# Kernel tuning notes

Measured on AMD Instinct MI355X. Metric: run time of the kernel, lower is better.

## Reference

```python
import jax, jax.numpy as jnp
import numpy as np

B, N, NINP, NFEAT, H = 4096, 4096, 64, 32, 4


def setup_inputs() -> dict:
    key = jax.random.key(0)
    ks = jax.random.split(key, 8)
    s_in = 1.0 / np.sqrt(NINP)
    s_att = 1.0 / np.sqrt(2 * NFEAT)
    return {
        "X": jax.random.normal(ks[0], (B, NINP), jnp.float32),
        "G": jax.random.normal(ks[1], (N, NINP), jnp.float32),
        "A": jax.random.uniform(ks[2], (B, N), jnp.float32),  # additive mask
        "W": jax.random.uniform(ks[3], (H, NINP, NFEAT), jnp.float32, -s_in, s_in),
        "b": jax.random.uniform(ks[4], (H, NFEAT), jnp.float32, -s_in, s_in),
        "a_src": jax.random.uniform(ks[5], (H, NFEAT), jnp.float32, -s_att, s_att),
        "a_dst": jax.random.uniform(ks[6], (H, NFEAT), jnp.float32, -s_att, s_att),
        "att_b": jax.random.uniform(ks[7], (H,), jnp.float32, -s_att, s_att),
    }


def reference(X, G, A, W, b, a_src, a_dst, att_b):
    # Per-head linear transforms (all heads batched via einsum)
    WX = jnp.einsum("bi,hif->bhf", X, W) + b            # (B, H, F)
    WG = jnp.einsum("ni,hif->nhf", G, W) + b            # (N, H, F)
    # Decomposed concat-attention: a^T [WX_b ; WG_n] = a_src.WX_b + a_dst.WG_n
    s_src = jnp.einsum("bhf,hf->bh", WX, a_src)         # (B, H)
    s_dst = jnp.einsum("nhf,hf->nh", WG, a_dst)         # (N, H)
    e = s_src[:, :, None] + s_dst.T[None, :, :] + att_b[None, :, None]  # (B,H,N)
    att = jax.nn.softmax(e - A[:, None, :], axis=-1)    # adjacency-masked softmax
    # Dropout(0.5) is identity in eval mode (deterministic reference).
    out = jnp.einsum("bhn,nhf->bhf", att, WG)           # weighted aggregation
    out = jax.nn.relu(out)                              # activation before concat
    return out.reshape(out.shape[0], -1)                # (B, H*F) concat heads
```

## Files before the change

### kernel.cpp

```cpp
#include <hip/hip_runtime.h>
#include <stdint.h>

#define N_TOK 4096
#define D_IN  64
#define NF    32
#define NH    4
#define OUTW  (NH * NF)
#define NT    8
#define CHUNK 128
#define BT    32

typedef float        f32x4  __attribute__((ext_vector_type(4)));
typedef unsigned int uint4v __attribute__((ext_vector_type(4)));
typedef __bf16       bf16x8 __attribute__((ext_vector_type(8)));

union Frag { uint4v u; bf16x8 v; };

static __device__ __forceinline__ unsigned short f2bf_rne(float x) {
  unsigned u = __float_as_uint(x);
  u += 0x7fffu + ((u >> 16) & 1u);
  return (unsigned short)(u >> 16);
}

__global__ __launch_bounds__(128) void prep_kernel(
    const float* __restrict__ G, const float* __restrict__ W,
    const float* __restrict__ bias, const float* __restrict__ a_dst,
    unsigned short* __restrict__ PB) {
  __shared__ float gs[NT * D_IN];
  const int tid = threadIdx.x;
  const int n0  = blockIdx.x * NT;
  {
    const float4* src = (const float4*)(G + (size_t)n0 * D_IN);
    float4* dst = (float4*)gs;
    dst[tid] = src[tid];
  }
  __syncthreads();
  const int h = tid >> 5, f = tid & 31;
  float acc[NT];
  const float bb = bias[h * NF + f];
#pragma unroll
  for (int k = 0; k < NT; ++k) acc[k] = bb;
#pragma unroll
  for (int i = 0; i < D_IN; ++i) {
    const float wv = W[(h * D_IN + i) * NF + f];
#pragma unroll
    for (int k = 0; k < NT; ++k) acc[k] = fmaf(gs[k * D_IN + i], wv, acc[k]);
  }
  const float ad = a_dst[h * NF + f];
  float ev[NT];
#pragma unroll
  for (int k = 0; k < NT; ++k) {
    float s = acc[k] * ad;
    s += __shfl_xor(s, 1);  s += __shfl_xor(s, 2);  s += __shfl_xor(s, 4);
    s += __shfl_xor(s, 8);  s += __shfl_xor(s, 16);
    ev[k] = __expf(s);
  }
  const int t   = n0 >> 5;
  const int gq  = (n0 >> 3) & 3;
  const int set = (h << 1) | (f >> 4);
  const int col = f & 31 & 15;
  union { uint4 u4; unsigned short us[8]; } pk;
#pragma unroll
  for (int k = 0; k < NT; ++k) pk.us[k] = f2bf_rne(acc[k] * ev[k]);
  *(uint4*)(PB + (size_t)((((t * 9 + set) << 6) + (gq << 4) + col)) * 8) = pk.u4;
  if (f == 0) {
    union { uint4 u4; unsigned short us[8]; } pe;
#pragma unroll
    for (int k = 0; k < NT; ++k) pe.us[k] = f2bf_rne(ev[k]);
    *(uint4*)(PB + (size_t)((((t * 9 + 8) << 6) + (gq << 4) + h)) * 8) = pe.u4;
  }
  if (h == 0 && f >= 4 && f < 16) {
    uint4 z; z.x = 0u; z.y = 0u; z.z = 0u; z.w = 0u;
    *(uint4*)(PB + (size_t)((((t * 9 + 8) << 6) + (gq << 4) + f)) * 8) = z;
  }
}

template <int NS>
__global__ __launch_bounds__(512) void attn_kernel(
    const float* __restrict__ A, const unsigned short* __restrict__ PB,
    float* __restrict__ op, float* __restrict__ dp, float* __restrict__ out) {
  constexpr int NHALF  = N_TOK / NS;
  constexpr int NIT    = NHALF / CHUNK;
  constexpr int RINGSZ = BT * CHUNK * 2;
  __shared__ __align__(16) unsigned short ring[3 * BT * CHUNK];
  char* ringb = (char*)ring;

  const int tid  = threadIdx.x;
  const int lane = tid & 63;
  const int w    = tid >> 6;
  const int bid  = blockIdx.x;
  const int s    = bid & (NS - 1);
  const int b0   = (bid / NS) * BT;

  const int srow = tid >> 4, tp = tid & 15;
  const float* abase = A + (size_t)(b0 + srow) * N_TOK + s * NHALF + tp * 8;
  const int wb0 = srow * 256 + ((tp ^ (srow & 15)) << 4);

  const int rowm = lane & 15, g = lane >> 4;
  const char* pbb  = (const char*)PB + (size_t)s * (NHALF / 32) * 9216;
  const char* pown = pbb + (((w << 6) + lane) << 4);
  const char* pden = pbb + (((8 << 6) + lane) << 4);

  f32x4 acc0  = {0.f, 0.f, 0.f, 0.f}, acc1  = {0.f, 0.f, 0.f, 0.f};
  f32x4 accd0 = {0.f, 0.f, 0.f, 0.f}, accd1 = {0.f, 0.f, 0.f, 0.f};
  f32x4 aXa, aXb, aYa, aYb;
  Frag bo0, bo1, bo2, bo3, bd0, bd1, bd2, bd3;
  Frag co0, co1, co2, co3, cd0, cd1, cd2, cd3;
  int mR = 0, mW = 1;

#define LOADA2(d0, d1, cc) do {                                                \
    const float* ap_ = abase + (size_t)(cc) * CHUNK;                           \
    asm volatile("global_load_dwordx4 %0, %1, off"                            \
                 : "=v"(d0) : "v"(ap_) : "memory");                            \
    asm volatile("global_load_dwordx4 %0, %1, off"                            \
                 : "=v"(d1) : "v"(ap_ + 4) : "memory");                        \
  } while (0)
#define LOADBO(fr, cc, kk)                                                     \
  asm volatile("global_load_dwordx4 %0, %1, off"                              \
               : "=v"(fr.u)                                                    \
               : "v"(pown + (size_t)((cc) * 4 + (kk)) * 9216) : "memory")
#define LOADBD(fr, cc, kk)                                                     \
  asm volatile("global_load_dwordx4 %0, %1, off"                              \
               : "=v"(fr.u)                                                    \
               : "v"(pden + (size_t)((cc) * 4 + (kk)) * 9216) : "memory")

#define EXPP(AV0, AV1, mw) do {                                                \
    float x0 = __expf(-AV0[0]), x1 = __expf(-AV0[1]);                          \
    float x2 = __expf(-AV0[2]), x3 = __expf(-AV0[3]);                          \
    float x4 = __expf(-AV1[0]), x5 = __expf(-AV1[1]);                          \
    float x6 = __expf(-AV1[2]), x7 = __expf(-AV1[3]);                          \
    uint4v t_;                                                                 \
    t_[0] = __builtin_amdgcn_perm(__float_as_uint(x1), __float_as_uint(x0), 0x07060302u); \
    t_[1] = __builtin_amdgcn_perm(__float_as_uint(x3), __float_as_uint(x2), 0x07060302u); \
    t_[2] = __builtin_amdgcn_perm(__float_as_uint(x5), __float_as_uint(x4), 0x07060302u); \
    t_[3] = __builtin_amdgcn_perm(__float_as_uint(x7), __float_as_uint(x6), 0x07060302u); \
    *(uint4v*)(ringb + (mw) * RINGSZ + wb0) = t_;                              \
  } while (0)

#define MSTEP(rg, kk, FB, FD) do {                                             \
    Frag af_;                                                                  \
    af_.v = *(const bf16x8*)(ringb + mR * RINGSZ + ((rg) * 16 + rowm) * 256 +  \
                             ((((kk) * 4 + g) ^ rowm) << 4));                  \
    if ((rg) == 0) {                                                           \
      acc0  = __builtin_amdgcn_mfma_f32_16x16x32_bf16(af_.v, FB.v, acc0,  0, 0, 0); \
      accd0 = __builtin_amdgcn_mfma_f32_16x16x32_bf16(af_.v, FD.v, accd0, 0, 0, 0); \
    } else {                                                                   \
      acc1  = __builtin_amdgcn_mfma_f32_16x16x32_bf16(af_.v, FB.v, acc1,  0, 0, 0); \
      accd1 = __builtin_amdgcn_mfma_f32_16x16x32_bf16(af_.v, FD.v, accd1, 0, 0, 0); \
    }                                                                          \
  } while (0)

#define ITER(cc, AC0, AC1, AN0, AN1, CO0, CO1, CO2, CO3, CD0, CD1, CD2, CD3,   \
             NO0, NO1, NO2, NO3, ND0, ND1, ND2, ND3) do {                      \
    { const int cb_ = ((cc) + 1 < NIT) ? (cc) + 1 : NIT - 1;                   \
      LOADBO(NO0, cb_, 0); LOADBO(NO1, cb_, 1);                                \
      LOADBO(NO2, cb_, 2); LOADBO(NO3, cb_, 3);                                \
      LOADBD(ND0, cb_, 0); LOADBD(ND1, cb_, 1);                                \
      LOADBD(ND2, cb_, 2); LOADBD(ND3, cb_, 3); }                              \
    { const int ca_ = ((cc) + 2 < NIT) ? (cc) + 2 : NIT - 1;                   \
      LOADA2(AN0, AN1, ca_); }                                                 \
    asm volatile("s_waitcnt vmcnt(10)" ::: "memory");                          \
    __builtin_amdgcn_sched_barrier(0);                                         \
    EXPP(AC0, AC1, mW);                                                        \
    asm volatile("s_waitcnt lgkmcnt(0)" ::: "memory");                         \
    __builtin_amdgcn_sched_barrier(0);                                         \
    __builtin_amdgcn_s_barrier();                                              \
    MSTEP(0, 0, CO0, CD0); MSTEP(1, 0, CO0, CD0);                              \
    MSTEP(0, 1, CO1, CD1); MSTEP(1, 1, CO1, CD1);                              \
    MSTEP(0, 2, CO2, CD2); MSTEP(1, 2, CO2, CD2);                              \
    MSTEP(0, 3, CO3, CD3); MSTEP(1, 3, CO3, CD3);                              \
    mR = mW; mW = (mW + 1 == 3) ? 0 : mW + 1;                                  \
  } while (0)

  LOADA2(aXa, aXb, 0);
  LOADBO(bo0, 0, 0); LOADBO(bo1, 0, 1); LOADBO(bo2, 0, 2); LOADBO(bo3, 0, 3);
  LOADBD(bd0, 0, 0); LOADBD(bd1, 0, 1); LOADBD(bd2, 0, 2); LOADBD(bd3, 0, 3);
  LOADA2(aYa, aYb, 1);
  asm volatile("s_waitcnt vmcnt(10)" ::: "memory");
  __builtin_amdgcn_sched_barrier(0);
  EXPP(aXa, aXb, 0);

#pragma unroll 1
  for (int i = 0; i < NIT; i += 2) {
    ITER(i,     aYa, aYb, aXa, aXb, bo0, bo1, bo2, bo3, bd0, bd1, bd2, bd3,
                                    co0, co1, co2, co3, cd0, cd1, cd2, cd3);
    ITER(i + 1, aXa, aXb, aYa, aYb, co0, co1, co2, co3, cd0, cd1, cd2, cd3,
                                    bo0, bo1, bo2, bo3, bd0, bd1, bd2, bd3);
  }

  asm volatile("s_waitcnt vmcnt(0)" ::: "memory");
  __builtin_amdgcn_sched_barrier(0);

  if (NS == 1) {
    const int hh = w >> 1;
#pragma unroll
    for (int r = 0; r < 4; ++r) {
      const float dn0 = __shfl(accd0[r], g * 16 + hh);
      const float o0 = acc0[r] / dn0;
      out[(size_t)(b0 + g * 4 + r) * OUTW + w * 16 + rowm] = o0 > 0.f ? o0 : 0.f;
      const float dn1 = __shfl(accd1[r], g * 16 + hh);
      const float o1 = acc1[r] / dn1;
      out[(size_t)(b0 + 16 + g * 4 + r) * OUTW + w * 16 + rowm] = o1 > 0.f ? o1 : 0.f;
    }
  } else {
    float* ob = op + (size_t)s * (N_TOK * OUTW) + (size_t)b0 * OUTW + w * 16 + rowm;
#pragma unroll
    for (int r = 0; r < 4; ++r) {
      ob[(size_t)(g * 4 + r) * OUTW]      = acc0[r];
      ob[(size_t)(16 + g * 4 + r) * OUTW] = acc1[r];
    }
    if (w == 0 && rowm < NH) {
#pragma unroll
      for (int r = 0; r < 4; ++r) {
        dp[((size_t)s * N_TOK + b0 + g * 4 + r) * NH + rowm]      = accd0[r];
        dp[((size_t)s * N_TOK + b0 + 16 + g * 4 + r) * NH + rowm] = accd1[r];
      }
    }
  }
#undef LOADA2
#undef LOADBO
#undef LOADBD
#undef EXPP
#undef MSTEP
#undef ITER
}

__global__ __launch_bounds__(256) void comb_kernel(
    const float* __restrict__ op, const float* __restrict__ dp,
    float* __restrict__ out, int NS) {
  const int idx4 = blockIdx.x * 256 + threadIdx.x;
  const int eb = idx4 >> 5;
  const int h  = ((idx4 << 2) & 127) >> 5;
  float4 o; o.x = 0.f; o.y = 0.f; o.z = 0.f; o.w = 0.f;
  float d = 0.f;
  for (int s2 = 0; s2 < NS; ++s2) {
    float4 vv = *(const float4*)(op + (size_t)s2 * (N_TOK * OUTW) + (size_t)idx4 * 4);
    o.x += vv.x; o.y += vv.y; o.z += vv.z; o.w += vv.w;
    d += dp[((size_t)s2 * N_TOK + eb) * NH + h];
  }
  const float r = 1.f / d;
  float4 res;
  res.x = fmaxf(o.x * r, 0.f);
  res.y = fmaxf(o.y * r, 0.f);
  res.z = fmaxf(o.z * r, 0.f);
  res.w = fmaxf(o.w * r, 0.f);
  *(float4*)(out + (size_t)idx4 * 4) = res;
}

extern "C" void kernel_launch(void* const* d_in, const int* in_sizes, int n_in,
                              void* d_out, int out_size, void* d_ws, size_t ws_size,
                              hipStream_t stream) {
  const float* G     = (const float*)d_in[1];
  const float* A     = (const float*)d_in[2];
  const float* W     = (const float*)d_in[3];
  const float* bias  = (const float*)d_in[4];
  const float* a_dst = (const float*)d_in[6];

  char* ws = (char*)d_ws;
  const size_t PBsz = (size_t)128 * 9 * 1024;
  const size_t per_split = (size_t)N_TOK * OUTW * 4 + (size_t)N_TOK * NH * 4;

  unsigned short* PB = (unsigned short*)ws;
  float* op = (float*)(ws + PBsz);
  float* outp = (float*)d_out;

  prep_kernel<<<N_TOK / NT, 128, 0, stream>>>(G, W, bias, a_dst, PB);
  if (ws_size >= PBsz + 4 * per_split) {
    float* dp = (float*)(ws + PBsz + 4 * (size_t)N_TOK * OUTW * 4);
    attn_kernel<4><<<(N_TOK / BT) * 4, 512, 0, stream>>>(A, PB, op, dp, nullptr);
    comb_kernel<<<(N_TOK * OUTW / 4) / 256, 256, 0, stream>>>(op, dp, outp, 4);
  } else if (ws_size >= PBsz + 2 * per_split) {
    float* dp = (float*)(ws + PBsz + 2 * (size_t)N_TOK * OUTW * 4);
    attn_kernel<2><<<(N_TOK / BT) * 2, 512, 0, stream>>>(A, PB, op, dp, nullptr);
    comb_kernel<<<(N_TOK * OUTW / 4) / 256, 256, 0, stream>>>(op, dp, outp, 2);
  } else {
    attn_kernel<1><<<N_TOK / BT, 512, 0, stream>>>(A, PB, nullptr, nullptr, outp);
  }
}
```

Baseline: 34.04 us.

## Compute softmax denominators with VALU FMAs instead of extra MFMAs

Removes the denominator MFMA path (4 extra global fragment loads and 8 extra MFMAs per chunk per wave). The per-head exp(s_dst) values are instead staged in LDS once per block, and each thread accumulates the denominator with scalar FMAs during the exp stage. The accumulation is then reduced via shuffles. This shrinks PB traffic and MFMA work, but adds 32 FMAs per thread per chunk, an LDS prologue copy, and extra LDS usage that could affect occupancy.

```diff
diff --git a/kernel.cpp b/kernel.cpp
--- a/kernel.cpp
+++ b/kernel.cpp
@@ -21,11 +21,17 @@
   u += 0x7fffu + ((u >> 16) & 1u);
   return (unsigned short)(u >> 16);
 }
+static __device__ __forceinline__ float bflo(unsigned x) {
+  return __uint_as_float(x << 16);
+}
+static __device__ __forceinline__ float bfhi(unsigned x) {
+  return __uint_as_float(x & 0xffff0000u);
+}
 
 __global__ __launch_bounds__(128) void prep_kernel(
     const float* __restrict__ G, const float* __restrict__ W,
     const float* __restrict__ bias, const float* __restrict__ a_dst,
-    unsigned short* __restrict__ PB) {
+    unsigned short* __restrict__ EDH, unsigned short* __restrict__ PB) {
   __shared__ float gs[NT * D_IN];
   const int tid = threadIdx.x;
   const int n0  = blockIdx.x * NT;
@@ -58,31 +64,30 @@
   const int t   = n0 >> 5;
   const int gq  = (n0 >> 3) & 3;
   const int set = (h << 1) | (f >> 4);
-  const int col = f & 31 & 15;
+  const int col = f & 15;
   union { uint4 u4; unsigned short us[8]; } pk;
 #pragma unroll
   for (int k = 0; k < NT; ++k) pk.us[k] = f2bf_rne(acc[k] * ev[k]);
-  *(uint4*)(PB + (size_t)((((t * 9 + set) << 6) + (gq << 4) + col)) * 8) = pk.u4;
+  *(uint4*)(PB + (size_t)((((t * 8 + set) << 6) + (gq << 4) + col)) * 8) = pk.u4;
   if (f == 0) {
     union { uint4 u4; unsigned short us[8]; } pe;
 #pragma unroll
     for (int k = 0; k < NT; ++k) pe.us[k] = f2bf_rne(ev[k]);
-    *(uint4*)(PB + (size_t)((((t * 9 + 8) << 6) + (gq << 4) + h)) * 8) = pe.u4;
-  }
-  if (h == 0 && f >= 4 && f < 16) {
-    uint4 z; z.x = 0u; z.y = 0u; z.z = 0u; z.w = 0u;
-    *(uint4*)(PB + (size_t)((((t * 9 + 8) << 6) + (gq << 4) + f)) * 8) = z;
+    *(uint4*)&EDH[(size_t)h * N_TOK + n0] = pe.u4;
   }
 }
 
 template <int NS>
 __global__ __launch_bounds__(512) void attn_kernel(
-    const float* __restrict__ A, const unsigned short* __restrict__ PB,
-    float* __restrict__ op, float* __restrict__ dp, float* __restrict__ out) {
+    const float* __restrict__ A, const unsigned short* __restrict__ EDH,
+    const unsigned short* __restrict__ PB, float* __restrict__ op,
+    float* __restrict__ dp, float* __restrict__ out) {
   constexpr int NHALF  = N_TOK / NS;
   constexpr int NIT    = NHALF / CHUNK;
   constexpr int RINGSZ = BT * CHUNK * 2;
   __shared__ __align__(16) unsigned short ring[3 * BT * CHUNK];
+  __shared__ __align__(16) unsigned short EDt[NH * NHALF];
+  __shared__ float denLds[BT * NH];
   char* ringb = (char*)ring;
 
   const int tid  = threadIdx.x;
@@ -97,15 +102,25 @@
   const int wb0 = srow * 256 + ((tp ^ (srow & 15)) << 4);
 
   const int rowm = lane & 15, g = lane >> 4;
-  const char* pbb  = (const char*)PB + (size_t)s * (NHALF / 32) * 9216;
+  const char* pbb  = (const char*)PB + (size_t)s * (NHALF / 32) * 8192;
   const char* pown = pbb + (((w << 6) + lane) << 4);
-  const char* pden = pbb + (((8 << 6) + lane) << 4);
-
-  f32x4 acc0  = {0.f, 0.f, 0.f, 0.f}, acc1  = {0.f, 0.f, 0.f, 0.f};
-  f32x4 accd0 = {0.f, 0.f, 0.f, 0.f}, accd1 = {0.f, 0.f, 0.f, 0.f};
+
+  {
+    const uint4* src = (const uint4*)EDH;
+    uint4* dst = (uint4*)EDt;
+    constexpr int tot = NH * NHALF / 8;
+#pragma unroll 1
+    for (int i = tid; i < tot; i += 512) {
+      const int hh = i / (NHALF / 8), k = i % (NHALF / 8);
+      dst[i] = src[hh * (N_TOK / 8) + s * (NHALF / 8) + k];
+    }
+  }
+  __syncthreads();
+
+  f32x4 acc0 = {0.f, 0.f, 0.f, 0.f}, acc1 = {0.f, 0.f, 0.f, 0.f};
+  f32x4 dsum = {0.f, 0.f, 0.f, 0.f};
   f32x4 aXa, aXb, aYa, aYb;
-  Frag bo0, bo1, bo2, bo3, bd0, bd1, bd2, bd3;
-  Frag co0, co1, co2, co3, cd0, cd1, cd2, cd3;
+  Frag bo0, bo1, bo2, bo3, co0, co1, co2, co3;
   int mR = 0, mW = 1;
 
 #define LOADA2(d0, d1, cc) do {                                                \
@@ -115,20 +130,55 @@
     asm volatile("global_load_dwordx4 %0, %1, off"                            \
                  : "=v"(d1) : "v"(ap_ + 4) : "memory");                        \
   } while (0)
-#define LOADBO(fr, cc, kk)                                                     \
+#define LOADB(fr, cc, kk)                                                      \
   asm volatile("global_load_dwordx4 %0, %1, off"                              \
                : "=v"(fr.u)                                                    \
-               : "v"(pown + (size_t)((cc) * 4 + (kk)) * 9216) : "memory")
-#define LOADBD(fr, cc, kk)                                                     \
-  asm volatile("global_load_dwordx4 %0, %1, off"                              \
-               : "=v"(fr.u)                                                    \
-               : "v"(pden + (size_t)((cc) * 4 + (kk)) * 9216) : "memory")
-
-#define EXPP(AV0, AV1, mw) do {                                                \
+               : "v"(pown + (size_t)((cc) * 4 + (kk)) * 8192) : "memory")
+
+#define EXPP(AV0, AV1, cchunk, mw) do {                                        \
     float x0 = __expf(-AV0[0]), x1 = __expf(-AV0[1]);                          \
     float x2 = __expf(-AV0[2]), x3 = __expf(-AV0[3]);                          \
     float x4 = __expf(-AV1[0]), x5 = __expf(-AV1[1]);                          \
     float x6 = __expf(-AV1[2]), x7 = __expf(-AV1[3]);                          \
+    if ((cchunk) < NIT) {                                                      \
+      const int eo_ = (cchunk) * CHUNK + tp * 8;                               \
+      uint4v e0_ = *(const uint4v*)&EDt[0 * NHALF + eo_];                      \
+      uint4v e1_ = *(const uint4v*)&EDt[1 * NHALF + eo_];                      \
+      uint4v e2_ = *(const uint4v*)&EDt[2 * NHALF + eo_];                      \
+      uint4v e3_ = *(const uint4v*)&EDt[3 * NHALF + eo_];                      \
+      dsum[0] = fmaf(x0, bflo(e0_[0]), dsum[0]);                               \
+      dsum[0] = fmaf(x1, bfhi(e0_[0]), dsum[0]);                               \
+      dsum[0] = fmaf(x2, bflo(e0_[1]), dsum[0]);                               \
+      dsum[0] = fmaf(x3, bfhi(e0_[1]), dsum[0]);                               \
+      dsum[0] = fmaf(x4, bflo(e0_[2]), dsum[0]);                               \
+      dsum[0] = fmaf(x5, bfhi(e0_[2]), dsum[0]);                               \
+      dsum[0] = fmaf(x6, bflo(e0_[3]), dsum[0]);                               \
+      dsum[0] = fmaf(x7, bfhi(e0_[3]), dsum[0]);                               \
+      dsum[1] = fmaf(x0, bflo(e1_[0]), dsum[1]);                               \
+      dsum[1] = fmaf(x1, bfhi(e1_[0]), dsum[1]);                               \
+      dsum[1] = fmaf(x2, bflo(e1_[1]), dsum[1]);                               \
+      dsum[1] = fmaf(x3, bfhi(e1_[1]), dsum[1]);                               \
+      dsum[1] = fmaf(x4, bflo(e1_[2]), dsum[1]);                               \
+      dsum[1] = fmaf(x5, bfhi(e1_[2]), dsum[1]);                               \
+      dsum[1] = fmaf(x6, bflo(e1_[3]), dsum[1]);                               \
+      dsum[1] = fmaf(x7, bfhi(e1_[3]), dsum[1]);                               \
+      dsum[2] = fmaf(x0, bflo(e2_[0]), dsum[2]);                               \
+      dsum[2] = fmaf(x1, bfhi(e2_[0]), dsum[2]);                               \
+      dsum[2] = fmaf(x2, bflo(e2_[1]), dsum[2]);                               \
+      dsum[2] = fmaf(x3, bfhi(e2_[1]), dsum[2]);                               \
+      dsum[2] = fmaf(x4, bflo(e2_[2]), dsum[2]);                               \
+      dsum[2] = fmaf(x5, bfhi(e2_[2]), dsum[2]);                               \
+      dsum[2] = fmaf(x6, bflo(e2_[3]), dsum[2]);                               \
+      dsum[2] = fmaf(x7, bfhi(e2_[3]), dsum[2]);                               \
+      dsum[3] = fmaf(x0, bflo(e3_[0]), dsum[3]);                               \
+      dsum[3] = fmaf(x1, bfhi(e3_[0]), dsum[3]);                               \
+      dsum[3] = fmaf(x2, bflo(e3_[1]), dsum[3]);                               \
+      dsum[3] = fmaf(x3, bfhi(e3_[1]), dsum[3]);                               \
+      dsum[3] = fmaf(x4, bflo(e3_[2]), dsum[3]);                               \
+      dsum[3] = fmaf(x5, bfhi(e3_[2]), dsum[3]);                               \
+      dsum[3] = fmaf(x6, bflo(e3_[3]), dsum[3]);                               \
+      dsum[3] = fmaf(x7, bfhi(e3_[3]), dsum[3]);                               \
+    }                                                                          \
     uint4v t_;                                                                 \
     t_[0] = __builtin_amdgcn_perm(__float_as_uint(x1), __float_as_uint(x0), 0x07060302u); \
     t_[1] = __builtin_amdgcn_perm(__float_as_uint(x3), __float_as_uint(x2), 0x07060302u); \
@@ -137,89 +187,91 @@
     *(uint4v*)(ringb + (mw) * RINGSZ + wb0) = t_;                              \
   } while (0)
 
-#define MSTEP(rg, kk, FB, FD) do {                                             \
+#define MSTEP(rg, kk, FB) do {                                                 \
     Frag af_;                                                                  \
     af_.v = *(const bf16x8*)(ringb + mR * RINGSZ + ((rg) * 16 + rowm) * 256 +  \
                              ((((kk) * 4 + g) ^ rowm) << 4));                  \
-    if ((rg) == 0) {                                                           \
-      acc0  = __builtin_amdgcn_mfma_f32_16x16x32_bf16(af_.v, FB.v, acc0,  0, 0, 0); \
-      accd0 = __builtin_amdgcn_mfma_f32_16x16x32_bf16(af_.v, FD.v, accd0, 0, 0, 0); \
-    } else {                                                                   \
-      acc1  = __builtin_amdgcn_mfma_f32_16x16x32_bf16(af_.v, FB.v, acc1,  0, 0, 0); \
-      accd1 = __builtin_amdgcn_mfma_f32_16x16x32_bf16(af_.v, FD.v, accd1, 0, 0, 0); \
-    }                                                                          \
+    if ((rg) == 0)                                                             \
+      acc0 = __builtin_amdgcn_mfma_f32_16x16x32_bf16(af_.v, FB.v, acc0, 0, 0, 0); \
+    else                                                                       \
+      acc1 = __builtin_amdgcn_mfma_f32_16x16x32_bf16(af_.v, FB.v, acc1, 0, 0, 0); \
   } while (0)
 
-#define ITER(cc, AC0, AC1, AN0, AN1, CO0, CO1, CO2, CO3, CD0, CD1, CD2, CD3,   \
-             NO0, NO1, NO2, NO3, ND0, ND1, ND2, ND3) do {                      \
+#define ITER(cc, AC0, AC1, AN0, AN1, CO0, CO1, CO2, CO3,                       \
+             NO0, NO1, NO2, NO3) do {                                          \
     { const int cb_ = ((cc) + 1 < NIT) ? (cc) + 1 : NIT - 1;                   \
-      LOADBO(NO0, cb_, 0); LOADBO(NO1, cb_, 1);                                \
-      LOADBO(NO2, cb_, 2); LOADBO(NO3, cb_, 3);                                \
-      LOADBD(ND0, cb_, 0); LOADBD(ND1, cb_, 1);                                \
-      LOADBD(ND2, cb_, 2); LOADBD(ND3, cb_, 3); }                              \
+      LOADB(NO0, cb_, 0); LOADB(NO1, cb_, 1);                                  \
+      LOADB(NO2, cb_, 2); LOADB(NO3, cb_, 3); }                                \
     { const int ca_ = ((cc) + 2 < NIT) ? (cc) + 2 : NIT - 1;                   \
       LOADA2(AN0, AN1, ca_); }                                                 \
-    asm volatile("s_waitcnt vmcnt(10)" ::: "memory");                          \
+    asm volatile("s_waitcnt vmcnt(6)" ::: "memory");                           \
     __builtin_amdgcn_sched_barrier(0);                                         \
-    EXPP(AC0, AC1, mW);                                                        \
+    EXPP(AC0, AC1, (cc) + 1, mW);                                              \
     asm volatile("s_waitcnt lgkmcnt(0)" ::: "memory");                         \
     __builtin_amdgcn_sched_barrier(0);                                         \
     __builtin_amdgcn_s_barrier();                                              \
-    MSTEP(0, 0, CO0, CD0); MSTEP(1, 0, CO0, CD0);                              \
-    MSTEP(0, 1, CO1, CD1); MSTEP(1, 1, CO1, CD1);                              \
-    MSTEP(0, 2, CO2, CD2); MSTEP(1, 2, CO2, CD2);                              \
-    MSTEP(0, 3, CO3, CD3); MSTEP(1, 3, CO3, CD3);                              \
+    MSTEP(0, 0, CO0); MSTEP(1, 0, CO0);                                        \
+    MSTEP(0, 1, CO1); MSTEP(1, 1, CO1);                                        \
+    MSTEP(0, 2, CO2); MSTEP(1, 2, CO2);                                        \
+    MSTEP(0, 3, CO3); MSTEP(1, 3, CO3);                                        \
     mR = mW; mW = (mW + 1 == 3) ? 0 : mW + 1;                                  \
   } while (0)
 
   LOADA2(aXa, aXb, 0);
-  LOADBO(bo0, 0, 0); LOADBO(bo1, 0, 1); LOADBO(bo2, 0, 2); LOADBO(bo3, 0, 3);
-  LOADBD(bd0, 0, 0); LOADBD(bd1, 0, 1); LOADBD(bd2, 0, 2); LOADBD(bd3, 0, 3);
+  LOADB(bo0, 0, 0); LOADB(bo1, 0, 1); LOADB(bo2, 0, 2); LOADB(bo3, 0, 3);
   LOADA2(aYa, aYb, 1);
-  asm volatile("s_waitcnt vmcnt(10)" ::: "memory");
+  asm volatile("s_waitcnt vmcnt(6)" ::: "memory");
   __builtin_amdgcn_sched_barrier(0);
-  EXPP(aXa, aXb, 0);
+  EXPP(aXa, aXb, 0, 0);
 
 #pragma unroll 1
   for (int i = 0; i < NIT; i += 2) {
-    ITER(i,     aYa, aYb, aXa, aXb, bo0, bo1, bo2, bo3, bd0, bd1, bd2, bd3,
-                                    co0, co1, co2, co3, cd0, cd1, cd2, cd3);
-    ITER(i + 1, aXa, aXb, aYa, aYb, co0, co1, co2, co3, cd0, cd1, cd2, cd3,
-                                    bo0, bo1, bo2, bo3, bd0, bd1, bd2, bd3);
+    ITER(i,     aYa, aYb, aXa, aXb, bo0, bo1, bo2, bo3, co0, co1, co2, co3);
+    ITER(i + 1, aXa, aXb, aYa, aYb, co0, co1, co2, co3, bo0, bo1, bo2, bo3);
   }
 
   asm volatile("s_waitcnt vmcnt(0)" ::: "memory");
   __builtin_amdgcn_sched_barrier(0);
 
+#pragma unroll
+  for (int m = 1; m <= 8; m <<= 1) {
+    dsum[0] += __shfl_xor(dsum[0], m);
+    dsum[1] += __shfl_xor(dsum[1], m);
+    dsum[2] += __shfl_xor(dsum[2], m);
+    dsum[3] += __shfl_xor(dsum[3], m);
+  }
+
   if (NS == 1) {
+    if (tp == 0) {
+      float4 dv; dv.x = dsum[0]; dv.y = dsum[1]; dv.z = dsum[2]; dv.w = dsum[3];
+      *(float4*)&denLds[srow * NH] = dv;
+    }
+    __syncthreads();
     const int hh = w >> 1;
 #pragma unroll
     for (int r = 0; r < 4; ++r) {
-      const float dn0 = __shfl(accd0[r], g * 16 + hh);
-      const float o0 = acc0[r] / dn0;
-      out[(size_t)(b0 + g * 4 + r) * OUTW + w * 16 + rowm] = o0 > 0.f ? o0 : 0.f;
-      const float dn1 = __shfl(accd1[r], g * 16 + hh);
-      const float o1 = acc1[r] / dn1;
-      out[(size_t)(b0 + 16 + g * 4 + r) * OUTW + w * 16 + rowm] = o1 > 0.f ? o1 : 0.f;
+      const int rr = g * 4 + r;
+      float o;
+      o = acc0[r] / denLds[rr * NH + hh];
+      out[(size_t)(b0 + rr) * OUTW + w * 16 + rowm] = o > 0.f ? o : 0.f;
+      o = acc1[r] / denLds[(16 + rr) * NH + hh];
+      out[(size_t)(b0 + 16 + rr) * OUTW + w * 16 + rowm] = o > 0.f ? o : 0.f;
     }
   } else {
+    if (tp == 0) {
+      float4 dv; dv.x = dsum[0]; dv.y = dsum[1]; dv.z = dsum[2]; dv.w = dsum[3];
+      *(float4*)&dp[((size_t)s * N_TOK + b0 + srow) * NH] = dv;
+    }
     float* ob = op + (size_t)s * (N_TOK * OUTW) + (size_t)b0 * OUTW + w * 16 + rowm;
 #pragma unroll
     for (int r = 0; r < 4; ++r) {
-      ob[(size_t)(g * 4 + r) * OUTW]      = acc0[r];
-      ob[(size_t)(16 + g * 4 + r) * OUTW] = acc1[r];
-    }
-    if (w == 0 && rowm < NH) {
-#pragma unroll
-      for (int r = 0; r < 4; ++r) {
-        dp[((size_t)s * N_TOK + b0 + g * 4 + r) * NH + rowm]      = accd0[r];
-        dp[((size_t)s * N_TOK + b0 + 16 + g * 4 + r) * NH + rowm] = accd1[r];
-      }
+      const int rr = g * 4 + r;
+      ob[(size_t)rr * OUTW]        = acc0[r];
+      ob[(size_t)(16 + rr) * OUTW] = acc1[r];
     }
   }
 #undef LOADA2
-#undef LOADBO
-#undef LOADBD
+#undef LOADB
 #undef EXPP
 #undef MSTEP
 #undef ITER
@@ -257,23 +309,26 @@
   const float* a_dst = (const float*)d_in[6];
 
   char* ws = (char*)d_ws;
-  const size_t PBsz = (size_t)128 * 9 * 1024;
+  const size_t PBsz = (size_t)128 * 8 * 1024;
+  const size_t EDsz = (size_t)N_TOK * NH * 2;
+  const size_t base = PBsz + EDsz;
   const size_t per_split = (size_t)N_TOK * OUTW * 4 + (size_t)N_TOK * NH * 4;
 
-  unsigned short* PB = (unsigned short*)ws;
-  float* op = (float*)(ws + PBsz);
+  unsigned short* PB  = (unsigned short*)ws;
+  unsigned short* EDH = (unsigned short*)(ws + PBsz);
+  float* op = (float*)(ws + base);
   float* outp = (float*)d_out;
 
-  prep_kernel<<<N_TOK / NT, 128, 0, stream>>>(G, W, bias, a_dst, PB);
-  if (ws_size >= PBsz + 4 * per_split) {
-    float* dp = (float*)(ws + PBsz + 4 * (size_t)N_TOK * OUTW * 4);
-    attn_kernel<4><<<(N_TOK / BT) * 4, 512, 0, stream>>>(A, PB, op, dp, nullptr);
+  prep_kernel<<<N_TOK / NT, 128, 0, stream>>>(G, W, bias, a_dst, EDH, PB);
+  if (ws_size >= base + 4 * per_split) {
+    float* dp = (float*)(ws + base + 4 * (size_t)N_TOK * OUTW * 4);
+    attn_kernel<4><<<(N_TOK / BT) * 4, 512, 0, stream>>>(A, EDH, PB, op, dp, nullptr);
     comb_kernel<<<(N_TOK * OUTW / 4) / 256, 256, 0, stream>>>(op, dp, outp, 4);
-  } else if (ws_size >= PBsz + 2 * per_split) {
-    float* dp = (float*)(ws + PBsz + 2 * (size_t)N_TOK * OUTW * 4);
-    attn_kernel<2><<<(N_TOK / BT) * 2, 512, 0, stream>>>(A, PB, op, dp, nullptr);
+  } else if (ws_size >= base + 2 * per_split) {
+    float* dp = (float*)(ws + base + 2 * (size_t)N_TOK * OUTW * 4);
+    attn_kernel<2><<<(N_TOK / BT) * 2, 512, 0, stream>>>(A, EDH, PB, op, dp, nullptr);
     comb_kernel<<<(N_TOK * OUTW / 4) / 256, 256, 0, stream>>>(op, dp, outp, 2);
   } else {
-    attn_kernel<1><<<N_TOK / BT, 512, 0, stream>>>(A, PB, nullptr, nullptr, outp);
-  }
-}
+    attn_kernel<1><<<N_TOK / BT, 512, 0, stream>>>(A, EDH, PB, nullptr, nullptr, outp);
+  }
+}
```

Result: faster. 31.76 us (-6.7%).
